# Optimization experiments

Hardware: AMD Instinct MI355X
Metric: run time of the kernel (lower is better)

The kernel has to match this reference:

```python
import jax, jax.numpy as jnp
import numpy as np

N_HEADS = 16
D_HEAD = 64
D_MODEL = 1024


def apply_rotary_emb(t, cos, sin):
    # t: (B, H, T, D), cos/sin: (T, D//2) -> half-split rotation
    d2 = t.shape[-1] // 2
    t1, t2 = t[..., :d2], t[..., d2:]
    cos = cos[None, None, :, :]
    sin = sin[None, None, :, :]
    return jnp.concatenate([t1 * cos - t2 * sin, t1 * sin + t2 * cos], axis=-1)


def setup_inputs() -> dict:
    key = jax.random.key(0)
    ks = jax.random.split(key, 8)
    B, T = 2, 2048
    x = jax.random.normal(ks[0], (B, T, D_MODEL), dtype=jnp.float32)
    # rotary cache built from standard inv-freq schedule
    inv_freq = 1.0 / (10000.0 ** (jnp.arange(0, D_HEAD, 2, dtype=jnp.float32) / D_HEAD))
    ang = jnp.arange(T, dtype=jnp.float32)[:, None] * inv_freq[None, :]  # (T, D/2)
    cos, sin = jnp.cos(ang), jnp.sin(ang)
    s = 1.0 / np.sqrt(D_MODEL)
    W_q = jax.random.normal(ks[1], (D_MODEL, N_HEADS * D_HEAD), dtype=jnp.float32) * s
    W_k = jax.random.normal(ks[2], (D_MODEL, N_HEADS * D_HEAD), dtype=jnp.float32) * s
    W_v = jax.random.normal(ks[3], (D_MODEL, N_HEADS * D_HEAD), dtype=jnp.float32) * s
    W_out = jax.random.normal(ks[4], (N_HEADS * D_HEAD, D_MODEL), dtype=jnp.float32) * s
    return {"x": x, "cos": cos, "sin": sin, "W_q": W_q, "W_k": W_k, "W_v": W_v, "W_out": W_out}


def reference(x, cos, sin, W_q, W_k, W_v, W_out):
    B, T, _ = x.shape
    def split_heads(t):
        return t.reshape(B, T, N_HEADS, D_HEAD).transpose(0, 2, 1, 3)  # (B,H,T,D)
    q = split_heads(x @ W_q)
    k = split_heads(x @ W_k)
    v = split_heads(x @ W_v)
    q = apply_rotary_emb(q, cos, sin)
    k = apply_rotary_emb(k, cos, sin)
    scores = jnp.einsum('bhqd,bhkd->bhqk', q, k) / np.sqrt(D_HEAD).astype(np.float32)
    causal = jnp.triu(jnp.ones((T, T), dtype=bool), k=1)
    scores = jnp.where(causal[None, None], -jnp.inf, scores)
    attn = jax.nn.softmax(scores, axis=-1)
    z = jnp.einsum('bhqk,bhkd->bhqd', attn, v)
    z = z.transpose(0, 2, 1, 3).reshape(B, T, N_HEADS * D_HEAD)
    return z @ W_out
```

## Files before the change

### kernel.cpp

```cpp
#include <hip/hip_runtime.h>

typedef __attribute__((ext_vector_type(4))) float f32x4;
typedef __attribute__((ext_vector_type(8))) short short8;
typedef __attribute__((ext_vector_type(8))) unsigned short u16x8;
typedef __attribute__((ext_vector_type(4))) unsigned short u16x4;
typedef __attribute__((ext_vector_type(2))) unsigned int u32x2;

#define D_MODEL 1024
#define NHEADS 16
#define T_SEQ 2048
#define M_TOT 4096

__device__ __forceinline__ unsigned short f2bf(float f) {
    union { float f; unsigned int u; } v; v.f = f;
    return (unsigned short)((v.u + 0x7fffu + ((v.u >> 16) & 1u)) >> 16);
}
__device__ __forceinline__ float bf2f(unsigned short b) {
    union { unsigned int u; float f; } v; v.u = ((unsigned int)b) << 16;
    return v.f;
}
__device__ __forceinline__ unsigned int cvtpk_bf16(float lo, float hi) {
    unsigned int r;
    asm("v_cvt_pk_bf16_f32 %0, %1, %2" : "=v"(r) : "v"(lo), "v"(hi));
    return r;
}

#define GLD0(dst, addr) \
    asm volatile("global_load_dwordx4 %0, %1, off" : "=v"(dst) : "v"(addr) : "memory")
#define WAITV0() do { asm volatile("s_waitcnt vmcnt(0)" ::: "memory"); \
                      __builtin_amdgcn_sched_barrier(0); } while (0)
#define LBAR() do { asm volatile("s_waitcnt lgkmcnt(0)" ::: "memory"); \
                    __builtin_amdgcn_s_barrier(); \
                    __builtin_amdgcn_sched_barrier(0); } while (0)

#define GLDS16(gp, lp) \
    __builtin_amdgcn_global_load_lds((const __attribute__((address_space(1))) void*)(gp), \
                                     (__attribute__((address_space(3))) void*)(lp), 16, 0, 0)

__global__ __launch_bounds__(256) void prep_kernel(const float* __restrict__ X,
                                                   unsigned short* __restrict__ Xb,
                                                   const float* __restrict__ W0,
                                                   const float* __restrict__ W1,
                                                   const float* __restrict__ W2,
                                                   const float* __restrict__ W3,
                                                   unsigned short* __restrict__ Wt0) {
    __shared__ float tile[64][65];
    const int z = blockIdx.z;
    if (z >= 4) {
        const int blk = (z - 4) * 256 + blockIdx.y * 16 + blockIdx.x;
        const int i = (blk * 256 + threadIdx.x) * 4;
        const float4 v = *(const float4*)(X + i);
        u16x4 r;
        r.x = f2bf(v.x); r.y = f2bf(v.y); r.z = f2bf(v.z); r.w = f2bf(v.w);
        *(u16x4*)(Xb + i) = r;
        return;
    }
    const float* W = (z == 0) ? W0 : (z == 1) ? W1 : (z == 2) ? W2 : W3;
    unsigned short* Wt = Wt0 + (size_t)z * D_MODEL * D_MODEL;
    const int n0 = blockIdx.x * 64, k0 = blockIdx.y * 64;
    for (int i = threadIdx.x; i < 4096; i += 256) {
        const int r = i >> 6, c = i & 63;
        tile[r][c] = W[(size_t)(k0 + r) * D_MODEL + n0 + c];
    }
    __syncthreads();
    for (int i = threadIdx.x; i < 4096; i += 256) {
        const int r = i >> 6, c = i & 63;
        Wt[(size_t)(n0 + r) * D_MODEL + k0 + c] = f2bf(tile[c][r]);
    }
}

#define TN_G 128
#define BK_G 64

template<int MI, int OUTMODE>
__global__ __launch_bounds__(256) void gemm_kernel(
    const unsigned short* __restrict__ A,
    const unsigned short* __restrict__ Bt0,
    void* __restrict__ Cout0,
    const float* __restrict__ cosp,
    const float* __restrict__ sinp,
    float* __restrict__ Kmax)
{
    constexpr int TMc = MI * 32;
    constexpr int NCHA = TMc / 8;
    constexpr int NCHB = TN_G / 8;
    __shared__ unsigned short sA[2][TMc * 64];
    __shared__ unsigned short sB[2][TN_G * 64];

    const int tid = threadIdx.x;
    const int wid = tid >> 6;
    const int lane = tid & 63;
    const int quad = lane >> 4;
    const int l16 = lane & 15;
    const int wm = wid >> 1, wn = wid & 1;
    const int m0 = blockIdx.x * TMc, n0 = blockIdx.y * TN_G;
    const int z = blockIdx.z;
    const unsigned short* Bt = Bt0 + (size_t)z * D_MODEL * D_MODEL;
    const int r8 = lane >> 3;
    const int c8 = lane & 7;
    const int cswz = (c8 ^ r8) * 8;
    const int rx = l16 & 7;

    f32x4 acc[MI][4] = {};

    auto STAGE = [&](int b, int k0) {
        for (int ch = wid; ch < NCHA + NCHB; ch += 4) {
            if (ch < NCHA)
                GLDS16(A + (size_t)(m0 + ch * 8 + r8) * D_MODEL + k0 + cswz,
                       &sA[b][ch * 512]);
            else
                GLDS16(Bt + (size_t)(n0 + (ch - NCHA) * 8 + r8) * D_MODEL + k0 + cswz,
                       &sB[b][(ch - NCHA) * 512]);
        }
    };
    auto COMPUTE = [&](int b) {
        #pragma unroll
        for (int ks = 0; ks < 2; ++ks) {
            const int sx = ((ks * 4 + quad) ^ rx) * 8;
            short8 af[MI], bf[4];
            #pragma unroll
            for (int i = 0; i < MI; ++i)
                af[i] = *(const short8*)&sA[b][(wm * (MI * 16) + i * 16 + l16) * 64 + sx];
            #pragma unroll
            for (int i = 0; i < 4; ++i)
                bf[i] = *(const short8*)&sB[b][(wn * 64 + i * 16 + l16) * 64 + sx];
            #pragma unroll
            for (int mi = 0; mi < MI; ++mi)
                #pragma unroll
                for (int ni = 0; ni < 4; ++ni)
                    acc[mi][ni] = __builtin_amdgcn_mfma_f32_16x16x32_bf16(af[mi], bf[ni], acc[mi][ni], 0, 0, 0);
        }
    };

    STAGE(0, 0);
    WAITV0();
    LBAR();
    for (int kk = 0; kk < D_MODEL / BK_G; ++kk) {
        if (kk + 1 < D_MODEL / BK_G) STAGE((kk + 1) & 1, (kk + 1) * BK_G);
        COMPUTE(kk & 1);
        WAITV0();
        LBAR();
    }

    if constexpr (OUTMODE == 0) {
        float* C = (float*)Cout0;
        #pragma unroll
        for (int mi = 0; mi < MI; ++mi) {
            const int mb = m0 + wm * (MI * 16) + mi * 16 + quad * 4;
            #pragma unroll
            for (int ni = 0; ni < 4; ++ni) {
                const int n = n0 + wn * 64 + ni * 16 + l16;
                #pragma unroll
                for (int r = 0; r < 4; ++r)
                    C[(size_t)(mb + r) * D_MODEL + n] = acc[mi][ni][r];
            }
        }
    } else {
        unsigned short* O = (unsigned short*)Cout0 + (size_t)z * M_TOT * D_MODEL;
        const int h = (n0 + wn * 64) >> 6;
        if (z == 2) {
            #pragma unroll
            for (int mi = 0; mi < MI; ++mi) {
                const int mb = m0 + wm * (MI * 16) + mi * 16 + quad * 4;
                const int b = mb >> 11, t = mb & (T_SEQ - 1);
                #pragma unroll
                for (int ni = 0; ni < 4; ++ni) {
                    const int d = ni * 16 + l16;
                    u16x4 pk;
                    #pragma unroll
                    for (int r = 0; r < 4; ++r) pk[r] = f2bf(acc[mi][ni][r]);
                    *(u16x4*)(O + ((size_t)(b * NHEADS + h) * 64 + d) * T_SEQ + t) = pk;
                }
            }
        } else {
            if (z == 1) {
                float mx = 0.f;
                #pragma unroll
                for (int mi = 0; mi < MI; ++mi)
                    #pragma unroll
                    for (int r = 0; r < 4; ++r) {
                        float s = 0.f;
                        #pragma unroll
                        for (int ni = 0; ni < 4; ++ni) s += acc[mi][ni][r] * acc[mi][ni][r];
                        s += __shfl_xor(s, 1); s += __shfl_xor(s, 2);
                        s += __shfl_xor(s, 4); s += __shfl_xor(s, 8);
                        mx = fmaxf(mx, s);
                    }
                mx = fmaxf(mx, __shfl_xor(mx, 16));
                mx = fmaxf(mx, __shfl_xor(mx, 32));
                if (lane == 0) {
                    const int b = m0 >> 11;
                    const int slot = ((m0 >> 7) & 15) * 2 + wm;
                    Kmax[(size_t)(b * NHEADS + h) * 32 + slot] = __builtin_sqrtf(mx);
                }
            }
            const float qs = (z == 0) ? 0.125f : 1.0f;
            #pragma unroll
            for (int mi = 0; mi < MI; ++mi) {
                #pragma unroll
                for (int r = 0; r < 4; ++r) {
                    const int m = m0 + wm * (MI * 16) + mi * 16 + quad * 4 + r;
                    const int b = m >> 11, t = m & (T_SEQ - 1);
                    const size_t rowoff = ((size_t)(b * NHEADS + h) * T_SEQ + t) * 64;
                    #pragma unroll
                    for (int ni = 0; ni < 2; ++ni) {
                        const int d = ni * 16 + l16;
                        const float c = cosp[t * 32 + d], s = sinp[t * 32 + d];
                        const float x1 = acc[mi][ni][r], x2 = acc[mi][ni + 2][r];
                        O[rowoff + d]      = f2bf((x1 * c - x2 * s) * qs);
                        O[rowoff + d + 32] = f2bf((x1 * s + x2 * c) * qs);
                    }
                }
            }
        }
    }
}

#define LOG2E 1.44269504f

struct AttnSmem {
    union {
        unsigned short kv[2][4][4096];
        float comb[4][64][34];
    } u;
    unsigned short P[8][16 * 64];
};

__global__ __launch_bounds__(512, 2) void attn_kernel(
    const unsigned short* __restrict__ Q,
    const unsigned short* __restrict__ Kg,
    const unsigned short* __restrict__ Vt,
    const float* __restrict__ Kseg,
    unsigned short* __restrict__ Z)
{
    __shared__ AttnSmem sm;

    const int tid = threadIdx.x;
    const int wid = tid >> 6;
    const int w4 = wid & 3;
    const int half = wid >> 2;
    const int lane = tid & 63;
    const int quad = lane >> 4;
    const int l16 = lane & 15;
    const int srow = tid >> 3;
    const int sslot = tid & 7;
    const int wslot = sslot ^ (srow & 7);
    const int sxK = (quad ^ (l16 & 7)) << 3;
    const int ph8 = (l16 & 7) << 3;

    const int flat = blockIdx.x + 16 * blockIdx.y;
    const int xcd = flat & 7, idx = flat >> 3;
    const int bh = xcd * 4 + (idx & 3);
    const int x = idx >> 2;

    const int qA = x, qB = 31 - x;
    const int jend = 31 - x;

    const unsigned short* Qp = Q + (size_t)bh * T_SEQ * 64;
    const unsigned short* Kp = Kg + (size_t)bh * T_SEQ * 64;
    const unsigned short* Vp = Vt + (size_t)bh * 64 * T_SEQ;

    short8 aqA[2], aqB[2];
    {
        const unsigned short* qr = Qp + (size_t)(qA * 64 + w4 * 16 + l16) * 64 + quad * 8;
        aqA[0] = *(const short8*)(qr);
        aqA[1] = *(const short8*)(qr + 32);
        qr = Qp + (size_t)(qB * 64 + w4 * 16 + l16) * 64 + quad * 8;
        aqB[0] = *(const short8*)(qr);
        aqB[1] = *(const short8*)(qr + 32);
    }

    float kmx = 0.f;
    #pragma unroll
    for (int i = 0; i < 32; ++i) kmx = fmaxf(kmx, Kseg[bh * 32 + i]);

    float mQA, mQB;
    {
        float nqA = 0.f, nqB = 0.f;
        #pragma unroll
        for (int i = 0; i < 2; ++i)
            #pragma unroll
            for (int e = 0; e < 8; ++e) {
                const float fa = bf2f((unsigned short)aqA[i][e]);
                const float fb = bf2f((unsigned short)aqB[i][e]);
                nqA += fa * fa; nqB += fb * fb;
            }
        nqA += __shfl_xor(nqA, 16); nqA += __shfl_xor(nqA, 32);
        nqB += __shfl_xor(nqB, 16); nqB += __shfl_xor(nqB, 32);
        mQA = __builtin_sqrtf(nqA) * kmx * LOG2E;
        mQB = __builtin_sqrtf(nqB) * kmx * LOG2E;
    }

    auto tile_pack = [&](f32x4 (&s)[4], float mQ, float& lsum, bool msk,
                         unsigned short* Pw) {
        if (msk) {
            #pragma unroll
            for (int nt = 0; nt < 4; ++nt)
                #pragma unroll
                for (int r = 0; r < 4; ++r)
                    if (nt * 16 + quad * 4 + r > w4 * 16 + l16) s[nt][r] = -1e30f;
        }
        #pragma unroll
        for (int nt = 0; nt < 4; ++nt) {
            const float p0 = __builtin_exp2f(s[nt][0] * LOG2E - mQ);
            const float p1 = __builtin_exp2f(s[nt][1] * LOG2E - mQ);
            const float p2 = __builtin_exp2f(s[nt][2] * LOG2E - mQ);
            const float p3 = __builtin_exp2f(s[nt][3] * LOG2E - mQ);
            lsum += (p0 + p1) + (p2 + p3);
            const unsigned int w0 = cvtpk_bf16(p0, p1);
            const unsigned int w1 = cvtpk_bf16(p2, p3);
            *(u32x2*)&Pw[l16 * 64 + ((nt * 16 + quad * 4) ^ ph8)] = (u32x2){w0, w1};
        }
    };

    f32x4 oA[4] = {}, oB[4] = {};
    float lA = 0.f, lB = 0.f;
    unsigned short* Pw = &sm.P[wid][0];

    short8 stg[4];
    auto ISSUE = [&](int t) {
        const int j0 = 2 * t, j1 = j0 + 1;
        GLD0(stg[0], Kp + (size_t)j0 * 4096 + tid * 8);
        GLD0(stg[1], Vp + (size_t)srow * 2048 + j0 * 64 + sslot * 8);
        GLD0(stg[2], Kp + (size_t)j1 * 4096 + tid * 8);
        GLD0(stg[3], Vp + (size_t)srow * 2048 + j1 * 64 + sslot * 8);
    };
    auto WRITE = [&](int b) {
        const int dst = srow * 64 + (wslot << 3);
        *(short8*)&sm.u.kv[b][0][dst] = stg[0];
        *(short8*)&sm.u.kv[b][1][dst] = stg[1];
        *(short8*)&sm.u.kv[b][2][dst] = stg[2];
        *(short8*)&sm.u.kv[b][3][dst] = stg[3];
    };

    auto COMPUTE = [&](int j, int b) {
        if (j > jend) return;
        const bool doA = (j <= x);
        const unsigned short* sKb = &sm.u.kv[b][half * 2][0];
        const unsigned short* sVb = &sm.u.kv[b][half * 2 + 1][0];
        f32x4 sA[4] = {}, sB[4] = {};
        __builtin_amdgcn_s_setprio(1);
        #pragma unroll
        for (int nt = 0; nt < 4; ++nt) {
            const int rb = (nt * 16 + l16) * 64;
            const short8 k0 = *(const short8*)&sKb[rb + sxK];
            const short8 k1 = *(const short8*)&sKb[rb + (sxK ^ 32)];
            if (doA) {
                sA[nt] = __builtin_amdgcn_mfma_f32_16x16x32_bf16(k0, aqA[0], sA[nt], 0, 0, 0);
                sA[nt] = __builtin_amdgcn_mfma_f32_16x16x32_bf16(k1, aqA[1], sA[nt], 0, 0, 0);
            }
            sB[nt] = __builtin_amdgcn_mfma_f32_16x16x32_bf16(k0, aqB[0], sB[nt], 0, 0, 0);
            sB[nt] = __builtin_amdgcn_mfma_f32_16x16x32_bf16(k1, aqB[1], sB[nt], 0, 0, 0);
        }
        __builtin_amdgcn_s_setprio(0);
        short8 pfA0 = {}, pfA1 = {};
        if (doA) {
            tile_pack(sA, mQA, lA, j == x, Pw);
            asm volatile("s_waitcnt lgkmcnt(0)" ::: "memory");
            pfA0 = *(const short8*)&Pw[l16 * 64 + ((quad * 8) ^ ph8)];
            pfA1 = *(const short8*)&Pw[l16 * 64 + ((32 + quad * 8) ^ ph8)];
        }
        tile_pack(sB, mQB, lB, j == jend, Pw);
        asm volatile("s_waitcnt lgkmcnt(0)" ::: "memory");
        const short8 pfB0 = *(const short8*)&Pw[l16 * 64 + ((quad * 8) ^ ph8)];
        const short8 pfB1 = *(const short8*)&Pw[l16 * 64 + ((32 + quad * 8) ^ ph8)];
        __builtin_amdgcn_s_setprio(1);
        #pragma unroll
        for (int dt = 0; dt < 4; ++dt) {
            const int rb = (dt * 16 + l16) * 64;
            const short8 v0 = *(const short8*)&sVb[rb + sxK];
            const short8 v1 = *(const short8*)&sVb[rb + (sxK ^ 32)];
            if (doA) {
                oA[dt] = __builtin_amdgcn_mfma_f32_16x16x32_bf16(pfA0, v0, oA[dt], 0, 0, 0);
                oA[dt] = __builtin_amdgcn_mfma_f32_16x16x32_bf16(pfA1, v1, oA[dt], 0, 0, 0);
            }
            oB[dt] = __builtin_amdgcn_mfma_f32_16x16x32_bf16(pfB0, v0, oB[dt], 0, 0, 0);
            oB[dt] = __builtin_amdgcn_mfma_f32_16x16x32_bf16(pfB1, v1, oB[dt], 0, 0, 0);
        }
        __builtin_amdgcn_s_setprio(0);
    };

    const int nr = (jend >> 1) + 1;
    ISSUE(0);
    WAITV0();
    WRITE(0);
    LBAR();
    for (int t = 0; t < nr; ++t) {
        const bool more = (t + 1 < nr);
        if (more) ISSUE(t + 1);
        COMPUTE(2 * t + half, t & 1);
        if (more) {
            WAITV0();
            WRITE((t + 1) & 1);
        }
        LBAR();
    }

    lA += __shfl_xor(lA, 16); lA += __shfl_xor(lA, 32);
    lB += __shfl_xor(lB, 16); lB += __shfl_xor(lB, 32);

    __syncthreads();
    if (half) {
        float* cb = &sm.u.comb[w4][lane][0];
        #pragma unroll
        for (int dt = 0; dt < 4; ++dt)
            #pragma unroll
            for (int r = 0; r < 4; ++r) {
                cb[dt * 4 + r]      = oA[dt][r];
                cb[16 + dt * 4 + r] = oB[dt][r];
            }
        cb[32] = lA; cb[33] = lB;
    }
    __syncthreads();
    if (half) return;

    {
        const float* cb = &sm.u.comb[w4][lane][0];
        #pragma unroll
        for (int dt = 0; dt < 4; ++dt)
            #pragma unroll
            for (int r = 0; r < 4; ++r) {
                oA[dt][r] += cb[dt * 4 + r];
                oB[dt][r] += cb[16 + dt * 4 + r];
            }
        lA += cb[32]; lB += cb[33];
    }

    const float iA = 1.f / lA, iB = 1.f / lB;
    float irA[4], irB[4];
    #pragma unroll
    for (int r = 0; r < 4; ++r) {
        const int src = (lane & 48) | (quad * 4 + r);
        irA[r] = __shfl(iA, src);
        irB[r] = __shfl(iB, src);
    }

    const int h = bh & 15, b = bh >> 4;
    #pragma unroll
    for (int dt = 0; dt < 4; ++dt)
        #pragma unroll
        for (int r = 0; r < 4; ++r) {
            const int rowA = qA * 64 + w4 * 16 + quad * 4 + r;
            const int rowB = qB * 64 + w4 * 16 + quad * 4 + r;
            const int col = h * 64 + dt * 16 + l16;
            Z[((size_t)b * T_SEQ + rowA) * D_MODEL + col] = f2bf(oA[dt][r] * irA[r]);
            Z[((size_t)b * T_SEQ + rowB) * D_MODEL + col] = f2bf(oB[dt][r] * irB[r]);
        }
}

extern "C" void kernel_launch(void* const* d_in, const int* in_sizes, int n_in,
                              void* d_out, int out_size, void* d_ws, size_t ws_size,
                              hipStream_t stream) {
    const float* x    = (const float*)d_in[0];
    const float* cosp = (const float*)d_in[1];
    const float* sinp = (const float*)d_in[2];
    const float* Wq   = (const float*)d_in[3];
    const float* Wk   = (const float*)d_in[4];
    const float* Wv   = (const float*)d_in[5];
    const float* Wo   = (const float*)d_in[6];

    char* w = (char*)d_ws;
    unsigned short* xb  = (unsigned short*)w; w += (size_t)M_TOT * D_MODEL * 2;
    unsigned short* wt  = (unsigned short*)w; w += (size_t)4 * D_MODEL * D_MODEL * 2;
    unsigned short* Qb  = (unsigned short*)w; w += (size_t)M_TOT * D_MODEL * 2;
    unsigned short* Kb  = (unsigned short*)w; w += (size_t)M_TOT * D_MODEL * 2;
    unsigned short* Vtb = (unsigned short*)w; w += (size_t)M_TOT * D_MODEL * 2;
    unsigned short* Zb  = (unsigned short*)w; w += (size_t)M_TOT * D_MODEL * 2;
    float*          Ks  = (float*)w;          w += 32 * 32 * sizeof(float);

    prep_kernel<<<dim3(16, 16, 20), 256, 0, stream>>>(x, xb, Wq, Wk, Wv, Wo, wt);

    gemm_kernel<4, 1><<<dim3(M_TOT / 128, D_MODEL / 128, 3), 256, 0, stream>>>(
        xb, wt, (void*)Qb, cosp, sinp, Ks);

    attn_kernel<<<dim3(16, 32), 512, 0, stream>>>(Qb, Kb, Vtb, Ks, Zb);

    gemm_kernel<4, 0><<<dim3(M_TOT / 128, D_MODEL / 128, 1), 256, 0, stream>>>(
        Zb, wt + (size_t)3 * D_MODEL * D_MODEL, d_out, nullptr, nullptr, nullptr);
}
```

Baseline: 205.5 us.

## Loop QKV projections inside one GEMM block and compute softmax row sums via MFMA

The QKV GEMM now runs the three projections sequentially inside each block instead of across a z grid dimension. This keeps the same A tile rows hot in L2/cache across Q, K and V but cuts the grid to a third. The attention kernel drops per-element scalar row-sum accumulation and cross-lane shuffles, and instead computes the softmax denominator by multiplying P with a ones vector using extra MFMAs. The trade is extra matrix work in exchange for fewer VALU ops, and the combine buffer grows to hold four partial sums per lane. The smaller GEMM grid (256 blocks) risks lower occupancy and less parallelism on the chip.

```diff
diff --git a/kernel.cpp b/kernel.cpp
--- a/kernel.cpp
+++ b/kernel.cpp
@@ -94,121 +94,124 @@
     const int l16 = lane & 15;
     const int wm = wid >> 1, wn = wid & 1;
     const int m0 = blockIdx.x * TMc, n0 = blockIdx.y * TN_G;
-    const int z = blockIdx.z;
-    const unsigned short* Bt = Bt0 + (size_t)z * D_MODEL * D_MODEL;
     const int r8 = lane >> 3;
     const int c8 = lane & 7;
     const int cswz = (c8 ^ r8) * 8;
     const int rx = l16 & 7;
 
-    f32x4 acc[MI][4] = {};
-
-    auto STAGE = [&](int b, int k0) {
-        for (int ch = wid; ch < NCHA + NCHB; ch += 4) {
-            if (ch < NCHA)
-                GLDS16(A + (size_t)(m0 + ch * 8 + r8) * D_MODEL + k0 + cswz,
-                       &sA[b][ch * 512]);
-            else
-                GLDS16(Bt + (size_t)(n0 + (ch - NCHA) * 8 + r8) * D_MODEL + k0 + cswz,
-                       &sB[b][(ch - NCHA) * 512]);
-        }
-    };
-    auto COMPUTE = [&](int b) {
-        #pragma unroll
-        for (int ks = 0; ks < 2; ++ks) {
-            const int sx = ((ks * 4 + quad) ^ rx) * 8;
-            short8 af[MI], bf[4];
-            #pragma unroll
-            for (int i = 0; i < MI; ++i)
-                af[i] = *(const short8*)&sA[b][(wm * (MI * 16) + i * 16 + l16) * 64 + sx];
-            #pragma unroll
-            for (int i = 0; i < 4; ++i)
-                bf[i] = *(const short8*)&sB[b][(wn * 64 + i * 16 + l16) * 64 + sx];
-            #pragma unroll
-            for (int mi = 0; mi < MI; ++mi)
-                #pragma unroll
-                for (int ni = 0; ni < 4; ++ni)
-                    acc[mi][ni] = __builtin_amdgcn_mfma_f32_16x16x32_bf16(af[mi], bf[ni], acc[mi][ni], 0, 0, 0);
-        }
-    };
-
-    STAGE(0, 0);
-    WAITV0();
-    LBAR();
-    for (int kk = 0; kk < D_MODEL / BK_G; ++kk) {
-        if (kk + 1 < D_MODEL / BK_G) STAGE((kk + 1) & 1, (kk + 1) * BK_G);
-        COMPUTE(kk & 1);
+    constexpr int NZ = (OUTMODE == 1) ? 3 : 1;
+    for (int z = 0; z < NZ; ++z) {
+        const unsigned short* Bt = Bt0 + (size_t)z * D_MODEL * D_MODEL;
+
+        f32x4 acc[MI][4] = {};
+
+        auto STAGE = [&](int b, int k0) {
+            for (int ch = wid; ch < NCHA + NCHB; ch += 4) {
+                if (ch < NCHA)
+                    GLDS16(A + (size_t)(m0 + ch * 8 + r8) * D_MODEL + k0 + cswz,
+                           &sA[b][ch * 512]);
+                else
+                    GLDS16(Bt + (size_t)(n0 + (ch - NCHA) * 8 + r8) * D_MODEL + k0 + cswz,
+                           &sB[b][(ch - NCHA) * 512]);
+            }
+        };
+        auto COMPUTE = [&](int b) {
+            #pragma unroll
+            for (int ks = 0; ks < 2; ++ks) {
+                const int sx = ((ks * 4 + quad) ^ rx) * 8;
+                short8 af[MI], bf[4];
+                #pragma unroll
+                for (int i = 0; i < MI; ++i)
+                    af[i] = *(const short8*)&sA[b][(wm * (MI * 16) + i * 16 + l16) * 64 + sx];
+                #pragma unroll
+                for (int i = 0; i < 4; ++i)
+                    bf[i] = *(const short8*)&sB[b][(wn * 64 + i * 16 + l16) * 64 + sx];
+                #pragma unroll
+                for (int mi = 0; mi < MI; ++mi)
+                    #pragma unroll
+                    for (int ni = 0; ni < 4; ++ni)
+                        acc[mi][ni] = __builtin_amdgcn_mfma_f32_16x16x32_bf16(af[mi], bf[ni], acc[mi][ni], 0, 0, 0);
+            }
+        };
+
+        STAGE(0, 0);
         WAITV0();
         LBAR();
-    }
-
-    if constexpr (OUTMODE == 0) {
-        float* C = (float*)Cout0;
-        #pragma unroll
-        for (int mi = 0; mi < MI; ++mi) {
-            const int mb = m0 + wm * (MI * 16) + mi * 16 + quad * 4;
-            #pragma unroll
-            for (int ni = 0; ni < 4; ++ni) {
-                const int n = n0 + wn * 64 + ni * 16 + l16;
-                #pragma unroll
-                for (int r = 0; r < 4; ++r)
-                    C[(size_t)(mb + r) * D_MODEL + n] = acc[mi][ni][r];
-            }
-        }
-    } else {
-        unsigned short* O = (unsigned short*)Cout0 + (size_t)z * M_TOT * D_MODEL;
-        const int h = (n0 + wn * 64) >> 6;
-        if (z == 2) {
+        for (int kk = 0; kk < D_MODEL / BK_G; ++kk) {
+            if (kk + 1 < D_MODEL / BK_G) STAGE((kk + 1) & 1, (kk + 1) * BK_G);
+            COMPUTE(kk & 1);
+            WAITV0();
+            LBAR();
+        }
+
+        if constexpr (OUTMODE == 0) {
+            float* C = (float*)Cout0;
             #pragma unroll
             for (int mi = 0; mi < MI; ++mi) {
                 const int mb = m0 + wm * (MI * 16) + mi * 16 + quad * 4;
-                const int b = mb >> 11, t = mb & (T_SEQ - 1);
                 #pragma unroll
                 for (int ni = 0; ni < 4; ++ni) {
-                    const int d = ni * 16 + l16;
-                    u16x4 pk;
+                    const int n = n0 + wn * 64 + ni * 16 + l16;
                     #pragma unroll
-                    for (int r = 0; r < 4; ++r) pk[r] = f2bf(acc[mi][ni][r]);
-                    *(u16x4*)(O + ((size_t)(b * NHEADS + h) * 64 + d) * T_SEQ + t) = pk;
+                    for (int r = 0; r < 4; ++r)
+                        C[(size_t)(mb + r) * D_MODEL + n] = acc[mi][ni][r];
                 }
             }
         } else {
-            if (z == 1) {
-                float mx = 0.f;
-                #pragma unroll
-                for (int mi = 0; mi < MI; ++mi)
+            unsigned short* O = (unsigned short*)Cout0 + (size_t)z * M_TOT * D_MODEL;
+            const int h = (n0 + wn * 64) >> 6;
+            if (z == 2) {
+                #pragma unroll
+                for (int mi = 0; mi < MI; ++mi) {
+                    const int mb = m0 + wm * (MI * 16) + mi * 16 + quad * 4;
+                    const int b = mb >> 11, t = mb & (T_SEQ - 1);
+                    #pragma unroll
+                    for (int ni = 0; ni < 4; ++ni) {
+                        const int d = ni * 16 + l16;
+                        u16x4 pk;
+                        #pragma unroll
+                        for (int r = 0; r < 4; ++r) pk[r] = f2bf(acc[mi][ni][r]);
+                        *(u16x4*)(O + ((size_t)(b * NHEADS + h) * 64 + d) * T_SEQ + t) = pk;
+                    }
+                }
+            } else {
+                if (z == 1) {
+                    float mx = 0.f;
+                    #pragma unroll
+                    for (int mi = 0; mi < MI; ++mi)
+                        #pragma unroll
+                        for (int r = 0; r < 4; ++r) {
+                            float s = 0.f;
+                            #pragma unroll
+                            for (int ni = 0; ni < 4; ++ni) s += acc[mi][ni][r] * acc[mi][ni][r];
+                            s += __shfl_xor(s, 1); s += __shfl_xor(s, 2);
+                            s += __shfl_xor(s, 4); s += __shfl_xor(s, 8);
+                            mx = fmaxf(mx, s);
+                        }
+                    mx = fmaxf(mx, __shfl_xor(mx, 16));
+                    mx = fmaxf(mx, __shfl_xor(mx, 32));
+                    if (lane == 0) {
+                        const int b = m0 >> 11;
+                        const int slot = ((m0 >> 7) & 15) * 2 + wm;
+                        Kmax[(size_t)(b * NHEADS + h) * 32 + slot] = __builtin_sqrtf(mx);
+                    }
+                }
+                const float qs = (z == 0) ? 0.125f : 1.0f;
+                #pragma unroll
+                for (int mi = 0; mi < MI; ++mi) {
                     #pragma unroll
                     for (int r = 0; r < 4; ++r) {
-                        float s = 0.f;
+                        const int m = m0 + wm * (MI * 16) + mi * 16 + quad * 4 + r;
+                        const int b = m >> 11, t = m & (T_SEQ - 1);
+                        const size_t rowoff = ((size_t)(b * NHEADS + h) * T_SEQ + t) * 64;
                         #pragma unroll
-                        for (int ni = 0; ni < 4; ++ni) s += acc[mi][ni][r] * acc[mi][ni][r];
-                        s += __shfl_xor(s, 1); s += __shfl_xor(s, 2);
-                        s += __shfl_xor(s, 4); s += __shfl_xor(s, 8);
-                        mx = fmaxf(mx, s);
-                    }
-                mx = fmaxf(mx, __shfl_xor(mx, 16));
-                mx = fmaxf(mx, __shfl_xor(mx, 32));
-                if (lane == 0) {
-                    const int b = m0 >> 11;
-                    const int slot = ((m0 >> 7) & 15) * 2 + wm;
-                    Kmax[(size_t)(b * NHEADS + h) * 32 + slot] = __builtin_sqrtf(mx);
-                }
-            }
-            const float qs = (z == 0) ? 0.125f : 1.0f;
-            #pragma unroll
-            for (int mi = 0; mi < MI; ++mi) {
-                #pragma unroll
-                for (int r = 0; r < 4; ++r) {
-                    const int m = m0 + wm * (MI * 16) + mi * 16 + quad * 4 + r;
-                    const int b = m >> 11, t = m & (T_SEQ - 1);
-                    const size_t rowoff = ((size_t)(b * NHEADS + h) * T_SEQ + t) * 64;
-                    #pragma unroll
-                    for (int ni = 0; ni < 2; ++ni) {
-                        const int d = ni * 16 + l16;
-                        const float c = cosp[t * 32 + d], s = sinp[t * 32 + d];
-                        const float x1 = acc[mi][ni][r], x2 = acc[mi][ni + 2][r];
-                        O[rowoff + d]      = f2bf((x1 * c - x2 * s) * qs);
-                        O[rowoff + d + 32] = f2bf((x1 * s + x2 * c) * qs);
+                        for (int ni = 0; ni < 2; ++ni) {
+                            const int d = ni * 16 + l16;
+                            const float c = cosp[t * 32 + d], s = sinp[t * 32 + d];
+                            const float x1 = acc[mi][ni][r], x2 = acc[mi][ni + 2][r];
+                            O[rowoff + d]      = f2bf((x1 * c - x2 * s) * qs);
+                            O[rowoff + d + 32] = f2bf((x1 * s + x2 * c) * qs);
+                        }
                     }
                 }
             }
@@ -221,7 +224,7 @@
 struct AttnSmem {
     union {
         unsigned short kv[2][4][4096];
-        float comb[4][64][34];
+        float comb[4][64][40];
     } u;
     unsigned short P[8][16 * 64];
 };
@@ -291,8 +294,11 @@
         mQB = __builtin_sqrtf(nqB) * kmx * LOG2E;
     }
 
-    auto tile_pack = [&](f32x4 (&s)[4], float mQ, float& lsum, bool msk,
-                         unsigned short* Pw) {
+    short8 bones;
+    #pragma unroll
+    for (int e = 0; e < 8; ++e) bones[e] = (short)0x3F80;
+
+    auto tile_pack = [&](f32x4 (&s)[4], float mQ, bool msk, unsigned short* Pw) {
         if (msk) {
             #pragma unroll
             for (int nt = 0; nt < 4; ++nt)
@@ -306,7 +312,6 @@
             const float p1 = __builtin_exp2f(s[nt][1] * LOG2E - mQ);
             const float p2 = __builtin_exp2f(s[nt][2] * LOG2E - mQ);
             const float p3 = __builtin_exp2f(s[nt][3] * LOG2E - mQ);
-            lsum += (p0 + p1) + (p2 + p3);
             const unsigned int w0 = cvtpk_bf16(p0, p1);
             const unsigned int w1 = cvtpk_bf16(p2, p3);
             *(u32x2*)&Pw[l16 * 64 + ((nt * 16 + quad * 4) ^ ph8)] = (u32x2){w0, w1};
@@ -314,7 +319,7 @@
     };
 
     f32x4 oA[4] = {}, oB[4] = {};
-    float lA = 0.f, lB = 0.f;
+    f32x4 lacA = {}, lacB = {};
     unsigned short* Pw = &sm.P[wid][0];
 
     short8 stg[4];
@@ -355,12 +360,12 @@
         __builtin_amdgcn_s_setprio(0);
         short8 pfA0 = {}, pfA1 = {};
         if (doA) {
-            tile_pack(sA, mQA, lA, j == x, Pw);
+            tile_pack(sA, mQA, j == x, Pw);
             asm volatile("s_waitcnt lgkmcnt(0)" ::: "memory");
             pfA0 = *(const short8*)&Pw[l16 * 64 + ((quad * 8) ^ ph8)];
             pfA1 = *(const short8*)&Pw[l16 * 64 + ((32 + quad * 8) ^ ph8)];
         }
-        tile_pack(sB, mQB, lB, j == jend, Pw);
+        tile_pack(sB, mQB, j == jend, Pw);
         asm volatile("s_waitcnt lgkmcnt(0)" ::: "memory");
         const short8 pfB0 = *(const short8*)&Pw[l16 * 64 + ((quad * 8) ^ ph8)];
         const short8 pfB1 = *(const short8*)&Pw[l16 * 64 + ((32 + quad * 8) ^ ph8)];
@@ -377,6 +382,12 @@
             oB[dt] = __builtin_amdgcn_mfma_f32_16x16x32_bf16(pfB0, v0, oB[dt], 0, 0, 0);
             oB[dt] = __builtin_amdgcn_mfma_f32_16x16x32_bf16(pfB1, v1, oB[dt], 0, 0, 0);
         }
+        if (doA) {
+            lacA = __builtin_amdgcn_mfma_f32_16x16x32_bf16(pfA0, bones, lacA, 0, 0, 0);
+            lacA = __builtin_amdgcn_mfma_f32_16x16x32_bf16(pfA1, bones, lacA, 0, 0, 0);
+        }
+        lacB = __builtin_amdgcn_mfma_f32_16x16x32_bf16(pfB0, bones, lacB, 0, 0, 0);
+        lacB = __builtin_amdgcn_mfma_f32_16x16x32_bf16(pfB1, bones, lacB, 0, 0, 0);
         __builtin_amdgcn_s_setprio(0);
     };
 
@@ -396,9 +407,6 @@
         LBAR();
     }
 
-    lA += __shfl_xor(lA, 16); lA += __shfl_xor(lA, 32);
-    lB += __shfl_xor(lB, 16); lB += __shfl_xor(lB, 32);
-
     __syncthreads();
     if (half) {
         float* cb = &sm.u.comb[w4][lane][0];
@@ -409,7 +417,8 @@
                 cb[dt * 4 + r]      = oA[dt][r];
                 cb[16 + dt * 4 + r] = oB[dt][r];
             }
-        cb[32] = lA; cb[33] = lB;
+        #pragma unroll
+        for (int r = 0; r < 4; ++r) { cb[32 + r] = lacA[r]; cb[36 + r] = lacB[r]; }
     }
     __syncthreads();
     if (half) return;
@@ -423,17 +432,13 @@
                 oA[dt][r] += cb[dt * 4 + r];
                 oB[dt][r] += cb[16 + dt * 4 + r];
             }
-        lA += cb[32]; lB += cb[33];
-    }
-
-    const float iA = 1.f / lA, iB = 1.f / lB;
+        #pragma unroll
+        for (int r = 0; r < 4; ++r) { lacA[r] += cb[32 + r]; lacB[r] += cb[36 + r]; }
+    }
+
     float irA[4], irB[4];
     #pragma unroll
-    for (int r = 0; r < 4; ++r) {
-        const int src = (lane & 48) | (quad * 4 + r);
-        irA[r] = __shfl(iA, src);
-        irB[r] = __shfl(iB, src);
-    }
+    for (int r = 0; r < 4; ++r) { irA[r] = 1.f / lacA[r]; irB[r] = 1.f / lacB[r]; }
 
     const int h = bh & 15, b = bh >> 4;
     #pragma unroll
@@ -470,7 +475,7 @@
 
     prep_kernel<<<dim3(16, 16, 20), 256, 0, stream>>>(x, xb, Wq, Wk, Wv, Wo, wt);
 
-    gemm_kernel<4, 1><<<dim3(M_TOT / 128, D_MODEL / 128, 3), 256, 0, stream>>>(
+    gemm_kernel<4, 1><<<dim3(M_TOT / 128, D_MODEL / 128, 1), 256, 0, stream>>>(
         xb, wt, (void*)Qb, cosp, sinp, Ks);
 
     attn_kernel<<<dim3(16, 32), 512, 0, stream>>>(Qb, Kb, Vtb, Ks, Zb);
```

Result: slower. 227.3 us (+10.6%).
